# Kernel optimization log

Measured on AMD Instinct MI355X. Metric: run time of the kernel, lower is better.

## Reference

```python
import jax, jax.numpy as jnp
import numpy as np

LAMBDA = 20.0   # lambda_val (blackbox-diff smoothing)
REG = 0.5       # reg
MAX_LABEL = 8   # labels drawn in [0, MAX_LABEL)


def _pairwise_dist(x):
    # x: [n, d] -> [n, n] euclidean distances (safe sqrt, exact 0 on diagonal)
    sq = jnp.sum(x * x, axis=-1)
    d2 = sq[:, None] + sq[None, :] - 2.0 * (x @ x.T)
    d2 = jnp.maximum(d2, 0.0)
    return jnp.where(d2 > 0, jnp.sqrt(jnp.where(d2 > 0, d2, 1.0)), 0.0)


def _single_linkage_adj(D, k):
    # Agglomerative (single-linkage) clustering of n points given [n,n] dists,
    # stopped at k clusters; returns [n,n] 0/1 cluster-adjacency matrix.
    n = D.shape[0]
    BIG = jnp.asarray(1e9, D.dtype)
    eye = jnp.eye(n, dtype=bool)
    Dw0 = jnp.where(eye, BIG, D)
    labels0 = jnp.arange(n)
    active0 = jnp.ones((n,), dtype=bool)

    def step(carry, _):
        Dw, labels, active = carry
        mask = active[:, None] & active[None, :] & ~eye
        flat = jnp.argmin(jnp.where(mask, Dw, BIG))
        i, j = flat // n, flat % n
        a = jnp.minimum(i, j)
        b = jnp.maximum(i, j)
        newrow = jnp.minimum(Dw[a], Dw[b])        # single linkage merge
        Dw = Dw.at[a, :].set(newrow).at[:, a].set(newrow)
        active = active.at[b].set(False)
        labels = jnp.where(labels == b, a, labels)
        return (Dw, labels, active), labels

    _, hist = jax.lax.scan(step, (Dw0, labels0, active0), None, length=n - 1)
    all_hist = jnp.concatenate([labels0[None, :], hist], axis=0)  # [n, n]; row m = labels after m merges (n-m clusters)
    lab = all_hist[n - k]
    return (lab[:, None] == lab[None, :]).astype(D.dtype)


def _solve(dists, ks):
    return jax.vmap(_single_linkage_adj)(dists, ks)


def setup_inputs() -> dict:
    key = jax.random.key(0)
    k1, k2, k3 = jax.random.split(key, 3)
    B, n, d = 256, 64, 768
    return {
        "query_embedding": jax.random.normal(k1, (B, d), dtype=jnp.float32),
        "psg_embeddings": jax.random.normal(k2, (B, n, d), dtype=jnp.float32),
        "labels": jax.random.randint(k3, (B, n), 0, MAX_LABEL, dtype=jnp.int64)
        if jax.config.jax_enable_x64 else jax.random.randint(k3, (B, n), 0, MAX_LABEL, dtype=jnp.int32),
    }


def reference(query_embedding, psg_embeddings, labels):
    # true_adj_mat: adj[i,j] = 1 iff i==j or label[i]==label[j] (diag is label-equal anyway)
    true_adj = (labels[:, :, None] == labels[:, None, :]).astype(jnp.float32)  # [B,n,n]
    # ks[i] = number of unique labels in sample i
    presence = (labels[..., None] == jnp.arange(MAX_LABEL)).any(axis=1)  # [B, MAX_LABEL]
    ks = presence.sum(axis=-1)

    scaled = query_embedding[:, None, :] * psg_embeddings            # [B,n,d]
    dists = jax.vmap(_pairwise_dist)(scaled)                          # [B,n,n]

    mean_similar = (dists * true_adj).sum() / true_adj.sum()
    mean_dissimilar = (dists * (1.0 - true_adj)).sum() / (1.0 - true_adj).sum()

    adj = _solve(dists, ks)                                           # OptimCluster forward
    err = adj * (1.0 - true_adj) + (1.0 - adj) * true_adj
    err_mean = err.mean(axis=0).sum()
    return err_mean + REG * (mean_similar - mean_dissimilar)
```

## Files before the change

### kernel.cpp

```cpp
#include <hip/hip_runtime.h>


#define NPTS 64
#define DIM 768
#define CH 128
#define NCH 6
#define NT 512
#define BIGF 1e9f
#define PGS 68

typedef __attribute__((ext_vector_type(8))) __bf16 bf16x8;
typedef __attribute__((ext_vector_type(4))) float f32x4;
typedef __attribute__((ext_vector_type(8))) unsigned short us8;

__device__ __forceinline__ void lds_fence() {
  asm volatile("s_waitcnt lgkmcnt(0)" ::: "memory");
  __builtin_amdgcn_sched_barrier(0);
}

__device__ __forceinline__ void split2(float x, unsigned short& h,
                                       unsigned short& m) {
  unsigned u = __float_as_uint(x);
  unsigned rb = (u + 0x7FFFu + ((u >> 16) & 1u)) & 0xFFFF0000u;
  h = (unsigned short)(rb >> 16);
  float r1 = x - __uint_as_float(rb);
  unsigned u1 = __float_as_uint(r1);
  unsigned rb1 = (u1 + 0x7FFFu + ((u1 >> 16) & 1u)) & 0xFFFF0000u;
  m = (unsigned short)(rb1 >> 16);
}

__device__ __forceinline__ void publish6(int v, unsigned long long (&m)[6]) {
  #pragma unroll
  for (int k = 0; k < 6; ++k) m[k] = __ballot(((v >> k) & 1) != 0);
}
__device__ __forceinline__ int extract6(const unsigned long long (&m)[6], int p) {
  int r = 0;
  #pragma unroll
  for (int k = 0; k < 6; ++k) r |= (int)((m[k] >> p) & 1ull) << k;
  return r;
}
__device__ __forceinline__ unsigned long long match6(int v) {
  unsigned long long m = ~0ull;
  #pragma unroll
  for (int bb = 0; bb < 6; ++bb) {
    unsigned long long mb = __ballot(((v >> bb) & 1) != 0);
    m &= (((v >> bb) & 1) != 0) ? mb : ~mb;
  }
  return m;
}

__device__ __forceinline__ void stage_chunk(
    unsigned short (*Hb)[NPTS][CH], const float4 (&pva)[2][2],
    const float4 (&qv)[2], int row0, int gran) {
  #pragma unroll
  for (int rr = 0; rr < 2; ++rr) {
    const int row = row0 + (rr << 5);
    float xs[8];
    xs[0] = pva[rr][0].x * qv[0].x; xs[1] = pva[rr][0].y * qv[0].y;
    xs[2] = pva[rr][0].z * qv[0].z; xs[3] = pva[rr][0].w * qv[0].w;
    xs[4] = pva[rr][1].x * qv[1].x; xs[5] = pva[rr][1].y * qv[1].y;
    xs[6] = pva[rr][1].z * qv[1].z; xs[7] = pva[rr][1].w * qv[1].w;
    us8 uh, um;
    #pragma unroll
    for (int e = 0; e < 8; ++e) {
      unsigned short hh, mm;
      split2(xs[e], hh, mm);
      uh[e] = hh; um[e] = mm;
    }
    const int p = gran ^ (row & 15);
    *reinterpret_cast<us8*>(&Hb[0][row][p << 3]) = uh;
    *reinterpret_cast<us8*>(&Hb[1][row][p << 3]) = um;
  }
}

__device__ __forceinline__ void mfma_chunk(
    const unsigned short (*Hb)[NPTS][CH], f32x4 (&acc)[2][2],
    int R, int C, int ksub, int lrow, int lhi) {
  #pragma unroll 1
  for (int ss = 0; ss < 2; ++ss) {
    const int s = ksub + (ss << 1);
    const int p = ((s << 2) + lhi) ^ lrow;
    bf16x8 fa[2][2], fb[2][2];
    #pragma unroll
    for (int v = 0; v < 2; ++v)
      #pragma unroll
      for (int tb = 0; tb < 2; ++tb) {
        const int row = (R << 5) + (tb << 4) + lrow;
        fa[v][tb] = *reinterpret_cast<const bf16x8*>(&Hb[v][row][p << 3]);
      }
    if (R != C) {
      #pragma unroll
      for (int v = 0; v < 2; ++v)
        #pragma unroll
        for (int tb = 0; tb < 2; ++tb) {
          const int row = (C << 5) + (tb << 4) + lrow;
          fb[v][tb] = *reinterpret_cast<const bf16x8*>(&Hb[v][row][p << 3]);
        }
    } else {
      #pragma unroll
      for (int v = 0; v < 2; ++v)
        #pragma unroll
        for (int tb = 0; tb < 2; ++tb) fb[v][tb] = fa[v][tb];
    }
    #pragma unroll
    for (int ti = 0; ti < 2; ++ti)
      #pragma unroll
      for (int tj = 0; tj < 2; ++tj) {
        acc[ti][tj] = __builtin_amdgcn_mfma_f32_16x16x32_bf16(fa[0][ti], fb[0][tj], acc[ti][tj], 0, 0, 0);
        acc[ti][tj] = __builtin_amdgcn_mfma_f32_16x16x32_bf16(fa[0][ti], fb[1][tj], acc[ti][tj], 0, 0, 0);
        acc[ti][tj] = __builtin_amdgcn_mfma_f32_16x16x32_bf16(fa[1][ti], fb[0][tj], acc[ti][tj], 0, 0, 0);
        acc[ti][tj] = __builtin_amdgcn_mfma_f32_16x16x32_bf16(fa[1][ti], fb[1][tj], acc[ti][tj], 0, 0, 0);
      }
  }
}

#define ISSUE_P(PV, cix) do {                                       \
    const int off_ = (cix) * CH;                                    \
    PV[0][0] = *(const float4*)(pr0 + off_);                        \
    PV[0][1] = *(const float4*)(pr0 + off_ + 4);                    \
    PV[1][0] = *(const float4*)(pr1 + off_);                        \
    PV[1][1] = *(const float4*)(pr1 + off_ + 4);                    \
  } while (0)

#define ISSUE_Q(QV, cix) do {                                       \
    const int off_ = (cix) * CH;                                    \
    QV[0] = *(const float4*)(qr + off_);                            \
    QV[1] = *(const float4*)(qr + off_ + 4);                        \
  } while (0)

__global__ __launch_bounds__(NT) void fused_kernel(
    const float* __restrict__ q,
    const float* __restrict__ psg,
    const int*   __restrict__ labels,
    float* __restrict__ simS_o, float* __restrict__ disS_o,
    int* __restrict__ simC_o, int* __restrict__ errC_o)
{
  __shared__ __align__(16) unsigned short Hml[2][2][NPTS][CH];
  __shared__ __align__(16) float PG[NPTS * PGS];
  __shared__ float diagf[NPTS];
  __shared__ int lab_s[NPTS];
  __shared__ __align__(8) unsigned long long ekey_s[NPTS];

  const int b = blockIdx.x;
  const int t = threadIdx.x;
  const int w = t >> 6;
  const int l = t & 63;

  const float* qb = q + (size_t)b * DIM;
  const float* pb = psg + (size_t)b * NPTS * DIM;

  const int row0 = t >> 4;
  const int gran = t & 15;
  const float* pr0 = pb + (size_t)row0 * DIM + (gran << 3);
  const float* pr1 = pr0 + 32 * DIM;
  const float* qr  = qb + (gran << 3);

  const int rw = w >> 1;
  const int R = rw >> 1, C = rw & 1;
  const int ksub = w & 1;
  const int lrow = l & 15;
  const int lhi  = l >> 4;

  f32x4 acc[2][2];
  {
    f32x4 z = {0.f, 0.f, 0.f, 0.f};
    acc[0][0] = z; acc[0][1] = z; acc[1][0] = z; acc[1][1] = z;
  }

  float4 pvaA[2][2], pvaB[2][2], qv[2];

  ISSUE_P(pvaA, 0);
  ISSUE_Q(qv, 0);
  ISSUE_P(pvaB, 1);
  stage_chunk(Hml[0], pvaA, qv, row0, gran);
  __syncthreads();

  #pragma unroll 1
  for (int cc = 0; cc < 3; ++cc) {
    if (cc < 2) ISSUE_P(pvaA, 2 * cc + 2);
    ISSUE_Q(qv, 2 * cc + 1);
    mfma_chunk(Hml[0], acc, R, C, ksub, lrow, lhi);
    stage_chunk(Hml[1], pvaB, qv, row0, gran);
    __syncthreads();
    if (cc < 2) {
      ISSUE_P(pvaB, 2 * cc + 3);
      ISSUE_Q(qv, 2 * cc + 2);
    }
    mfma_chunk(Hml[1], acc, R, C, ksub, lrow, lhi);
    if (cc < 2) stage_chunk(Hml[0], pvaA, qv, row0, gran);
    __syncthreads();
  }

  if (w & 1) {
    float* dst = PG + (rw << 10);
    #pragma unroll
    for (int ti = 0; ti < 2; ++ti)
      #pragma unroll
      for (int tj = 0; tj < 2; ++tj)
        *reinterpret_cast<f32x4*>(dst + (((ti << 1) + tj) << 8) + (l << 2)) = acc[ti][tj];
  }
  __syncthreads();
  if (!(w & 1)) {
    const float* src = PG + (rw << 10);
    #pragma unroll
    for (int ti = 0; ti < 2; ++ti)
      #pragma unroll
      for (int tj = 0; tj < 2; ++tj)
        acc[ti][tj] += *reinterpret_cast<const f32x4*>(src + (((ti << 1) + tj) << 8) + (l << 2));
  }
  __syncthreads();
  if (!(w & 1)) {
    #pragma unroll
    for (int ti = 0; ti < 2; ++ti)
      #pragma unroll
      for (int tj = 0; tj < 2; ++tj)
        #pragma unroll
        for (int reg = 0; reg < 4; ++reg) {
          const int grow = (R << 5) + (ti << 4) + (lhi << 2) + reg;
          const int gcol = (C << 5) + (tj << 4) + lrow;
          PG[grow * PGS + gcol] = acc[ti][tj][reg];
        }
  }
  __syncthreads();

  if (t < NPTS) diagf[t] = PG[t * PGS + t];
  __syncthreads();
  {
    const int r  = t >> 3;
    const int c0 = (t & 7) << 3;
    const float dr = diagf[r];
    #pragma unroll
    for (int e = 0; e < 8; ++e) {
      const int cc = c0 + e;
      const float gg = PG[r * PGS + cc];
      float d2 = dr + diagf[cc] - 2.f * gg;
      d2 = fmaxf(d2, 0.f);
      PG[r * PGS + cc] = (d2 > 0.f) ? sqrtf(d2) : 0.f;
    }
  }
  __syncthreads();
  if (w != 0) return;

  float drow[64];
  #pragma unroll
  for (int v4 = 0; v4 < 16; ++v4) {
    f32x4 x = *reinterpret_cast<const f32x4*>(&PG[l * PGS + (v4 << 2)]);
    drow[v4 * 4 + 0] = x[0]; drow[v4 * 4 + 1] = x[1];
    drow[v4 * 4 + 2] = x[2]; drow[v4 * 4 + 3] = x[3];
  }
  int tl = labels[b * NPTS + l];

  unsigned long long sMask = 0ull;
  int kcnt = 0;
  #pragma unroll
  for (int v = 0; v < 8; ++v) {
    unsigned long long mv = __ballot(tl == v);
    kcnt += (mv != 0ull) ? 1 : 0;
    if (tl == v) sMask = mv;
  }
  int simC = __popcll(sMask);
  const int merges = NPTS - kcnt;

  float simS = 0.f, disS = 0.f;
  #pragma unroll
  for (int j = 0; j < NPTS; ++j) {
    bool sim = (sMask >> j) & 1ull;
    simS += sim ? drow[j] : 0.f;
    disS += sim ? 0.f : drow[j];
  }

  unsigned long long same = 1ull << l;
  int repSlot = l;
  int ecnt = 0;

  #pragma unroll 1
  for (int rd = 0; rd < 6; ++rd) {
    float bva = BIGF, bvb = BIGF, bvc = BIGF, bvd = BIGF;
    int bja = 64, bjb = 64, bjc = 64, bjd = 64;
    #pragma unroll
    for (int j4 = 0; j4 < 16; ++j4) {
      const int j = j4 << 2;
      bool oa = !((same >> (j + 0)) & 1ull) && (drow[j + 0] < bva);
      bva = oa ? drow[j + 0] : bva; bja = oa ? j + 0 : bja;
      bool ob = !((same >> (j + 1)) & 1ull) && (drow[j + 1] < bvb);
      bvb = ob ? drow[j + 1] : bvb; bjb = ob ? j + 1 : bjb;
      bool oc = !((same >> (j + 2)) & 1ull) && (drow[j + 2] < bvc);
      bvc = oc ? drow[j + 2] : bvc; bjc = oc ? j + 2 : bjc;
      bool od = !((same >> (j + 3)) & 1ull) && (drow[j + 3] < bvd);
      bvd = od ? drow[j + 3] : bvd; bjd = od ? j + 3 : bjd;
    }
    float bv = bva; int bj = bja;
    if (bvb < bv || (bvb == bv && bjb < bj)) { bv = bvb; bj = bjb; }
    if (bvc < bv || (bvc == bv && bjc < bj)) { bv = bvc; bj = bjc; }
    if (bvd < bv || (bvd == bv && bjd < bj)) { bv = bvd; bj = bjd; }

    const unsigned bits = (bj < 64) ? __float_as_uint(bv) : 0xFFFFFFFFu;
    unsigned long long cand = same;
    unsigned minb = 0u;
    #pragma unroll
    for (int k = 31; k >= 0; --k) {
      unsigned long long mb = __ballot(((bits >> k) & 1u) != 0u);
      unsigned long long z = cand & ~mb;
      bool hz = (z != 0ull);
      cand = hz ? z : cand;
      minb = (minb << 1) | (hz ? 0u : 1u);
    }
    const bool valid = (minb != 0xFFFFFFFFu);
    const int wl = __ffsll((long long)cand) - 1;

    unsigned long long bjm[6]; publish6(bj, bjm);
    const int v_wl = extract6(bjm, wl);

    unsigned long long rpm[6]; publish6(repSlot, rpm);
    const int otherRep = extract6(rpm, v_wl);

    const bool isRoot = (l == repSlot);
    int ptr = repSlot;
    if (isRoot && valid) ptr = otherRep;

    unsigned long long pm[6]; publish6(ptr, pm);
    const int pd = extract6(pm, ptr);
    bool adder = false;
    if (isRoot && valid && ptr != l) {
      if (pd == l && l < ptr) ptr = l;
      else adder = true;
    }
    const unsigned long long A = __ballot(adder);
    if (adder)
      ekey_s[ecnt + __popcll(A & ((1ull << l) - 1ull))] =
          ((unsigned long long)minb << 12) |
          (unsigned long long)((wl << 6) | v_wl);
    ecnt += (int)__popcll(A);

    #pragma unroll 1
    for (int jj = 0; jj < 6; ++jj) {
      unsigned long long dm[6]; publish6(ptr, dm);
      const int p2 = extract6(dm, ptr);
      if (__ballot(p2 != ptr) == 0ull) break;
      ptr = p2;
    }
    same = match6(ptr);
    repSlot = __ffsll((long long)same) - 1;
    if (same == ~0ull) break;
  }
  lds_fence();

  const bool ehave = (l < ecnt);
  const unsigned long long my = ehave ? ekey_s[l] : ~0ull;
  int rank = 0;
  #pragma unroll 7
  for (int j = 0; j < 63; ++j) {
    unsigned long long kj = ekey_s[j];
    rank += (j < ecnt && kj < my) ? 1 : 0;
  }
  const bool kept = ehave && (rank < merges);
  const int eu = (int)((my >> 6) & 63);
  const int ev = (int)(my & 63);

  lab_s[l] = l;
  lds_fence();
  #pragma unroll 1
  for (int iter = 0; iter < 64; ++iter) {
    int m = 0; bool ch = false;
    if (kept) {
      const int lu = lab_s[eu], lv = lab_s[ev];
      m = min(lu, lv);
      ch = (m < lu) || (m < lv);
    }
    if (ch) {
      atomicMin(&lab_s[eu], m);
      atomicMin(&lab_s[ev], m);
    }
    lds_fence();
    const int la = lab_s[l];
    const int lb = lab_s[la];
    if (lb < la) lab_s[l] = lb;
    lds_fence();
    if (__ballot(ch) == 0ull) break;
  }
  const int cl = lab_s[l];

  const unsigned long long cMask = match6(cl);
  int ec2 = __popcll(cMask ^ sMask);

  #pragma unroll
  for (int off = 32; off; off >>= 1) {
    simS += __shfl_xor(simS, off);
    disS += __shfl_xor(disS, off);
    simC += __shfl_xor(simC, off);
    ec2  += __shfl_xor(ec2, off);
  }
  if (l == 0) {
    simS_o[b] = simS; disS_o[b] = disS;
    simC_o[b] = simC; errC_o[b] = ec2;
  }
}

__global__ __launch_bounds__(64) void finalize_kernel(
    const float* __restrict__ simS, const float* __restrict__ disS,
    const int* __restrict__ simC, const int* __restrict__ errC,
    float* __restrict__ out)
{
  const int l = threadIdx.x;
  double ss = 0.0, dd = 0.0, sc = 0.0, ec = 0.0;
  #pragma unroll
  for (int r = 0; r < 4; ++r) {
    int i = (r << 6) + l;
    ss += (double)simS[i];
    dd += (double)disS[i];
    sc += (double)simC[i];
    ec += (double)errC[i];
  }
  #pragma unroll
  for (int off = 32; off; off >>= 1) {
    ss += __shfl_xor(ss, off);
    dd += __shfl_xor(dd, off);
    sc += __shfl_xor(sc, off);
    ec += __shfl_xor(ec, off);
  }
  if (l == 0) {
    const double total = 256.0 * 4096.0;
    double ms = ss / sc;
    double md = dd / (total - sc);
    out[0] = (float)(ec / 256.0 + 0.5 * (ms - md));
  }
}

extern "C" void kernel_launch(void* const* d_in, const int* in_sizes, int n_in,
                              void* d_out, int out_size, void* d_ws, size_t ws_size,
                              hipStream_t stream) {
  const float* q      = (const float*)d_in[0];
  const float* psg    = (const float*)d_in[1];
  const int*   labels = (const int*)d_in[2];
  float* out = (float*)d_out;

  float* simS = (float*)d_ws;
  float* disS = simS + 256;
  int*   simC = (int*)(disS + 256);
  int*   errC = simC + 256;

  fused_kernel<<<256, NT, 0, stream>>>(q, psg, labels, simS, disS, simC, errC);
  finalize_kernel<<<1, 64, 0, stream>>>(simS, disS, simC, errC, out);
}
```

Before: 31.79 us.

## Split fused kernel into K-split Gram kernel and separate single-wave cluster kernel

```diff
diff --git a/kernel.cpp b/kernel.cpp
--- a/kernel.cpp
+++ b/kernel.cpp
@@ -4,10 +4,8 @@
 #define NPTS 64
 #define DIM 768
 #define CH 128
-#define NCH 6
 #define NT 512
 #define BIGF 1e9f
-#define PGS 68
 
 typedef __attribute__((ext_vector_type(8))) __bf16 bf16x8;
 typedef __attribute__((ext_vector_type(4))) float f32x4;
@@ -128,26 +126,22 @@
     QV[1] = *(const float4*)(qr + off_ + 4);                        \
   } while (0)
 
-__global__ __launch_bounds__(NT) void fused_kernel(
+__global__ __launch_bounds__(NT) void gram_kernel(
     const float* __restrict__ q,
     const float* __restrict__ psg,
-    const int*   __restrict__ labels,
-    float* __restrict__ simS_o, float* __restrict__ disS_o,
-    int* __restrict__ simC_o, int* __restrict__ errC_o)
+    float* __restrict__ Gp)
 {
   __shared__ __align__(16) unsigned short Hml[2][2][NPTS][CH];
-  __shared__ __align__(16) float PG[NPTS * PGS];
-  __shared__ float diagf[NPTS];
-  __shared__ int lab_s[NPTS];
-  __shared__ __align__(8) unsigned long long ekey_s[NPTS];
-
-  const int b = blockIdx.x;
+
+  const int blk = blockIdx.x;
+  const int s  = blk >> 1;
+  const int kh = blk & 1;
   const int t = threadIdx.x;
   const int w = t >> 6;
   const int l = t & 63;
 
-  const float* qb = q + (size_t)b * DIM;
-  const float* pb = psg + (size_t)b * NPTS * DIM;
+  const float* qb = q + (size_t)s * DIM + kh * 384;
+  const float* pb = psg + (size_t)s * NPTS * DIM + kh * 384;
 
   const int row0 = t >> 4;
   const int gran = t & 15;
@@ -175,24 +169,20 @@
   stage_chunk(Hml[0], pvaA, qv, row0, gran);
   __syncthreads();
 
-  #pragma unroll 1
-  for (int cc = 0; cc < 3; ++cc) {
-    if (cc < 2) ISSUE_P(pvaA, 2 * cc + 2);
-    ISSUE_Q(qv, 2 * cc + 1);
-    mfma_chunk(Hml[0], acc, R, C, ksub, lrow, lhi);
-    stage_chunk(Hml[1], pvaB, qv, row0, gran);
-    __syncthreads();
-    if (cc < 2) {
-      ISSUE_P(pvaB, 2 * cc + 3);
-      ISSUE_Q(qv, 2 * cc + 2);
-    }
-    mfma_chunk(Hml[1], acc, R, C, ksub, lrow, lhi);
-    if (cc < 2) stage_chunk(Hml[0], pvaA, qv, row0, gran);
-    __syncthreads();
-  }
-
+  ISSUE_P(pvaA, 2);
+  ISSUE_Q(qv, 1);
+  mfma_chunk(Hml[0], acc, R, C, ksub, lrow, lhi);
+  stage_chunk(Hml[1], pvaB, qv, row0, gran);
+  __syncthreads();
+  ISSUE_Q(qv, 2);
+  mfma_chunk(Hml[1], acc, R, C, ksub, lrow, lhi);
+  stage_chunk(Hml[0], pvaA, qv, row0, gran);
+  __syncthreads();
+  mfma_chunk(Hml[0], acc, R, C, ksub, lrow, lhi);
+
+  float* scr = (float*)&Hml[1][0][0][0];
   if (w & 1) {
-    float* dst = PG + (rw << 10);
+    float* dst = scr + (rw << 10);
     #pragma unroll
     for (int ti = 0; ti < 2; ++ti)
       #pragma unroll
@@ -201,15 +191,13 @@
   }
   __syncthreads();
   if (!(w & 1)) {
-    const float* src = PG + (rw << 10);
+    const float* src = scr + (rw << 10);
     #pragma unroll
     for (int ti = 0; ti < 2; ++ti)
       #pragma unroll
       for (int tj = 0; tj < 2; ++tj)
         acc[ti][tj] += *reinterpret_cast<const f32x4*>(src + (((ti << 1) + tj) << 8) + (l << 2));
-  }
-  __syncthreads();
-  if (!(w & 1)) {
+    float* Gb = Gp + (size_t)blk * NPTS * NPTS;
     #pragma unroll
     for (int ti = 0; ti < 2; ++ti)
       #pragma unroll
@@ -218,38 +206,47 @@
         for (int reg = 0; reg < 4; ++reg) {
           const int grow = (R << 5) + (ti << 4) + (lhi << 2) + reg;
           const int gcol = (C << 5) + (tj << 4) + lrow;
-          PG[grow * PGS + gcol] = acc[ti][tj][reg];
+          Gb[(grow << 6) + gcol] = acc[ti][tj][reg];
         }
   }
-  __syncthreads();
-
-  if (t < NPTS) diagf[t] = PG[t * PGS + t];
-  __syncthreads();
-  {
-    const int r  = t >> 3;
-    const int c0 = (t & 7) << 3;
-    const float dr = diagf[r];
-    #pragma unroll
-    for (int e = 0; e < 8; ++e) {
-      const int cc = c0 + e;
-      const float gg = PG[r * PGS + cc];
-      float d2 = dr + diagf[cc] - 2.f * gg;
-      d2 = fmaxf(d2, 0.f);
-      PG[r * PGS + cc] = (d2 > 0.f) ? sqrtf(d2) : 0.f;
-    }
-  }
-  __syncthreads();
-  if (w != 0) return;
+}
+
+__global__ __launch_bounds__(64) void cluster_kernel(
+    const float* __restrict__ Gp,
+    const int*   __restrict__ labels,
+    float* __restrict__ simS_o, float* __restrict__ disS_o,
+    int* __restrict__ simC_o, int* __restrict__ errC_o)
+{
+  __shared__ float diagf[NPTS];
+  __shared__ int lab_s[NPTS];
+  __shared__ __align__(8) unsigned long long ekey_s[NPTS];
+
+  const int b = blockIdx.x;
+  const int l = threadIdx.x;
+  const float* g0 = Gp + (size_t)(2 * b) * NPTS * NPTS + (l << 6);
+  const float* g1 = g0 + NPTS * NPTS;
+
+  float gr[64];
+  #pragma unroll
+  for (int v4 = 0; v4 < 16; ++v4) {
+    float4 a = *reinterpret_cast<const float4*>(g0 + (v4 << 2));
+    float4 c = *reinterpret_cast<const float4*>(g1 + (v4 << 2));
+    gr[v4 * 4 + 0] = a.x + c.x; gr[v4 * 4 + 1] = a.y + c.y;
+    gr[v4 * 4 + 2] = a.z + c.z; gr[v4 * 4 + 3] = a.w + c.w;
+  }
+  diagf[l] = gr[l];
+  lds_fence();
 
   float drow[64];
-  #pragma unroll
-  for (int v4 = 0; v4 < 16; ++v4) {
-    f32x4 x = *reinterpret_cast<const f32x4*>(&PG[l * PGS + (v4 << 2)]);
-    drow[v4 * 4 + 0] = x[0]; drow[v4 * 4 + 1] = x[1];
-    drow[v4 * 4 + 2] = x[2]; drow[v4 * 4 + 3] = x[3];
-  }
+  const float dl = gr[l];
+  #pragma unroll
+  for (int j = 0; j < NPTS; ++j) {
+    float d2 = dl + diagf[j] - 2.f * gr[j];
+    d2 = fmaxf(d2, 0.f);
+    drow[j] = (d2 > 0.f) ? sqrtf(d2) : 0.f;
+  }
+
   int tl = labels[b * NPTS + l];
-
   unsigned long long sMask = 0ull;
   int kcnt = 0;
   #pragma unroll
@@ -434,11 +431,13 @@
   const int*   labels = (const int*)d_in[2];
   float* out = (float*)d_out;
 
-  float* simS = (float*)d_ws;
+  float* Gp   = (float*)d_ws;
+  float* simS = Gp + 512 * NPTS * NPTS;
   float* disS = simS + 256;
   int*   simC = (int*)(disS + 256);
   int*   errC = simC + 256;
 
-  fused_kernel<<<256, NT, 0, stream>>>(q, psg, labels, simS, disS, simC, errC);
+  gram_kernel<<<512, NT, 0, stream>>>(q, psg, Gp);
+  cluster_kernel<<<256, 64, 0, stream>>>(Gp, labels, simS, disS, simC, errC);
   finalize_kernel<<<1, 64, 0, stream>>>(simS, disS, simC, errC, out);
 }
```

Result: slower. 39.41 us (+24.0%).
